# Kernel tuning notes

Measured on AMD Instinct MI355X. Metric: run time of the kernel, lower is better.

## Reference

```python
import jax, jax.numpy as jnp
import numpy as np

B, T, C, D = 4, 20, 128, 64
TD = T * D  # 1280; adaptor input dim = 2*TD = 2560


def setup_inputs() -> dict:
    key = jax.random.key(0)
    ks = jax.random.split(key, 12)

    def lin(k, out_d, in_d):
        return jax.random.normal(k, (out_d, in_d), jnp.float32) / np.float32(np.sqrt(in_d))

    return {
        "h": jax.random.normal(ks[0], (B, T, C, D), jnp.float32),
        "W1": lin(ks[1], 128, 2 * TD), "b1": jnp.zeros((128,), jnp.float32),
        "W2": lin(ks[2], 256, 128),   "b2": jnp.zeros((256,), jnp.float32),
        "W3": lin(ks[3], 64, 256),    "b3": jnp.zeros((64,), jnp.float32),
        "W4": lin(ks[4], 1, 64),      "b4": jnp.zeros((1,), jnp.float32),
        "A_a": jax.random.normal(ks[5], (C, C), jnp.float32) * 0.01,
        "A_m": jax.random.normal(ks[6], (C, C), jnp.float32) * 0.01,
        "W_add": lin(ks[7], D, D), "b_add": jnp.zeros((D,), jnp.float32),
        "W_mod": lin(ks[8], D, D), "b_mod": jnp.zeros((D,), jnp.float32),
        "beta1": jnp.float32(1.0), "beta2": jnp.float32(1.0), "beta3": jnp.float32(1.0),
    }


def reference(h, W1, b1, W2, b2, W3, b3, W4, b4, A_a, A_m,
              W_add, b_add, W_mod, b_mod, beta1, beta2, beta3):
    Bb, Tt, Cc, Dd = h.shape
    td = Tt * Dd
    # H^(u) flattened over time: (B, C, T*D)
    h_flat = jnp.transpose(h, (0, 2, 1, 3)).reshape(Bb, Cc, td)

    # Adaptor MLP on concat(H^u, H^v). First layer is linear on the concat,
    # so split W1 and broadcast-add instead of materializing (B,C,C,2*T*D).
    W1u, W1v = W1[:, :td], W1[:, td:]
    fu = h_flat @ W1u.T                      # (B, C, 128) contribution of u
    fv = h_flat @ W1v.T                      # (B, C, 128) contribution of v
    x = jax.nn.relu(fu[:, :, None, :] + fv[:, None, :, :] + b1)   # (B, Cu, Cv, 128)
    x = jax.nn.relu(jnp.einsum('buvk,mk->buvm', x, W2) + b2)       # (B, Cu, Cv, 256)
    x = jax.nn.relu(jnp.einsum('buvk,mk->buvm', x, W3) + b3)       # (B, Cu, Cv, 64)
    s = jax.nn.sigmoid(jnp.einsum('buvk,mk->buvm', x, W4) + b4)[..., 0]  # (B, C, C)

    # Add path: a_t^(v) = sum_u S^(u,v) * A_a^(u,v) * h_t^(u)
    w = s * A_a[None]                        # (B, Cu, Cv)
    a = jnp.einsum('buv,btud->btvd', w, h)   # (B, T, C, D)
    a = a @ W_add.T + b_add

    # Modulator path: m_t^(v) = (sum_u A_m^(u,v) h_t^(u)) * h_t^(v)
    m = jnp.einsum('uv,btud->btvd', A_m, h) * h
    m = m @ W_mod.T + b_mod

    return beta1 * h + beta2 * a + beta3 * m
```

## Files before the change

kernel.cpp:

```cpp
#include <hip/hip_runtime.h>
#include <cmath>

#define NB 4
#define NT 20
#define NC 128
#define ND 64
#define TD 1280

typedef short short8 __attribute__((ext_vector_type(8)));
typedef float f32x4 __attribute__((ext_vector_type(4)));

static __device__ __forceinline__ unsigned short f2bf(float f) {
  union { float f; unsigned int u; } v; v.f = f;
  unsigned int r = v.u + 0x7FFFu + ((v.u >> 16) & 1u);
  return (unsigned short)(r >> 16);
}

static __device__ __forceinline__ void conv16(const float* __restrict__ s,
                                              unsigned short* __restrict__ d) {
#pragma unroll
  for (int q = 0; q < 2; q++) {
    float4 f0 = *(const float4*)(s + q * 8);
    float4 f1 = *(const float4*)(s + q * 8 + 4);
    uint4 o;
    o.x = (unsigned)f2bf(f0.x) | ((unsigned)f2bf(f0.y) << 16);
    o.y = (unsigned)f2bf(f0.z) | ((unsigned)f2bf(f0.w) << 16);
    o.z = (unsigned)f2bf(f1.x) | ((unsigned)f2bf(f1.y) << 16);
    o.w = (unsigned)f2bf(f1.z) | ((unsigned)f2bf(f1.w) << 16);
    *(uint4*)(d + q * 8) = o;
  }
}

__global__ __launch_bounds__(256) void k_conv_a(
    const float* __restrict__ h, const float* __restrict__ W1,
    unsigned short* __restrict__ hbf, unsigned short* __restrict__ W1bf) {
  int blk = blockIdx.x, tid = threadIdx.x;
  if (blk < 160) {
    int bt = blk >> 1;
    int j = ((blk & 1) << 12) + tid * 16;
    int b = bt / 20;
    int c = j >> 6, d0 = j & 63;
    int t5 = bt - b * 20;
    conv16(h + (size_t)bt * 8192 + j,
           hbf + ((size_t)(b * NC + c)) * TD + t5 * 64 + d0);
  } else {
    size_t i = (size_t)(blk - 160) * 4096 + tid * 16;
    conv16(W1 + i, W1bf + i);
  }
}

__global__ __launch_bounds__(128) void k_fuv2(
    const unsigned short* __restrict__ hbf,
    const unsigned short* __restrict__ W1bf,
    const float* __restrict__ h, const float* __restrict__ W2,
    const float* __restrict__ W3, const float* __restrict__ A_m,
    const float* __restrict__ W_add, const float* __restrict__ W_mod,
    float* __restrict__ fuv,
    unsigned short* __restrict__ W2bf, unsigned short* __restrict__ W3bf,
    unsigned short* __restrict__ A_mTbf, unsigned short* __restrict__ W_addbf,
    unsigned short* __restrict__ W_modbf, unsigned short* __restrict__ hbfT) {
  __shared__ float hsl[128][65];
  int blk = blockIdx.x, tid = threadIdx.x;
  if (blk < 256) {
    int mtile = blk & 15;
    int ntile = blk >> 4;
    int lane = tid & 63;
    int w = tid >> 6;
    int lr = lane & 15, lhi = lane >> 4;
    int row = mtile * 32 + w * 16 + lr;
    const unsigned short* ap = hbf + (size_t)row * TD + lhi * 8;
    int n = ntile * 16 + lr;
    const unsigned short* bp =
        W1bf + (size_t)(n & 127) * (2 * TD) + (n >> 7) * TD + lhi * 8;
    f32x4 acc = (f32x4){0.f, 0.f, 0.f, 0.f};
#pragma unroll 4
    for (int kb = 0; kb < TD; kb += 32) {
      short8 a = *(const short8*)(ap + kb);
      short8 bv = *(const short8*)(bp + kb);
      acc = __builtin_amdgcn_mfma_f32_16x16x32_bf16(a, bv, acc, 0, 0, 0);
    }
    int m0 = mtile * 32 + w * 16 + lhi * 4;
#pragma unroll
    for (int r = 0; r < 4; r++)
      fuv[(size_t)(m0 + r) * 256 + n] = acc[r];
    return;
  }
  int cb = blk - 256;
  if (cb < 16) {
    size_t i = (size_t)cb * 2048 + tid * 16;
    conv16(W2 + i, W2bf + i);
  } else if (cb < 24) {
    size_t i = (size_t)(cb - 16) * 2048 + tid * 16;
    conv16(W3 + i, W3bf + i);
  } else if (cb < 32) {
    size_t base = (size_t)(cb - 24) * 2048 + tid * 16;
    unsigned short tmp[16];
#pragma unroll
    for (int i2 = 0; i2 < 16; i2++) {
      size_t idx = base + i2;
      int v = (int)(idx >> 7), u = (int)(idx & 127);
      tmp[i2] = f2bf(A_m[(size_t)u * 128 + v]);
    }
    *(uint4*)(A_mTbf + base) = *(uint4*)tmp;
    *(uint4*)(A_mTbf + base + 8) = *(uint4*)(tmp + 8);
  } else if (cb < 34) {
    size_t i = (size_t)(cb - 32) * 2048 + tid * 16;
    conv16(W_add + i, W_addbf + i);
  } else if (cb < 36) {
    size_t i = (size_t)(cb - 34) * 2048 + tid * 16;
    conv16(W_mod + i, W_modbf + i);
  } else {
    int bt = cb - 36;
    const float* hb = h + (size_t)bt * 8192;
    for (int i = tid; i < 8192; i += 128) hsl[i >> 6][i & 63] = hb[i];
    __syncthreads();
    unsigned short* ob = hbfT + (size_t)bt * 8192;
    for (int i = tid; i < 8192; i += 128) {
      int d = i >> 7, u = i & 127;
      ob[i] = f2bf(hsl[u][d]);
    }
  }
}

__global__ __launch_bounds__(256) void k_pair(
    const float* __restrict__ fuv, const float* __restrict__ b1,
    const unsigned short* __restrict__ W2bf, const float* __restrict__ b2,
    const unsigned short* __restrict__ W3bf, const float* __restrict__ b3,
    const float* __restrict__ W4, const float* __restrict__ b4,
    const float* __restrict__ A_a, unsigned short* __restrict__ wTbf) {
  int blk = blockIdx.x;
  int b = blk >> 7;
  int u = blk & 127;
  __shared__ char ycraw[4][4096];
  __shared__ char w2c[2][16384];
  __shared__ char w3c[2][8192];
  int t = threadIdx.x;
  int lane = t & 63;
  int w = t >> 6;
  int lr = lane & 15;
  int lhi = lane >> 4;
  int v0w = w * 32;
  int sw = (lr & 7) << 4;

  for (int s = w; s < 16; s += 4) {
    int o = s * 1024 + lane * 16;
    int row = o >> 8;
    int cbo = o & 255;
    const char* src = (const char*)W2bf + (size_t)row * 256 +
                      (cbo ^ ((row & 7) << 4));
    __builtin_amdgcn_global_load_lds(src, w2c[0] + s * 1024, 16, 0, 0);
  }
  for (int s = w; s < 8; s += 4) {
    int o = s * 1024 + lane * 16;
    int row = o >> 7;
    int cbo = o & 127;
    const char* src = (const char*)W3bf + (size_t)row * 512 +
                      (cbo ^ ((row & 7) << 4));
    __builtin_amdgcn_global_load_lds(src, w3c[0] + s * 1024, 16, 0, 0);
  }

  short8 xf[4][2];
  {
    const float* fu_base = fuv + ((size_t)(b * NC + u)) * 256;
#pragma unroll
    for (int ks = 0; ks < 4; ks++) {
      int k0 = ks * 32 + lhi * 8;
      float4 fua = *(const float4*)(fu_base + k0);
      float4 fub4 = *(const float4*)(fu_base + k0 + 4);
      float4 b1a = *(const float4*)(b1 + k0);
      float4 b1b = *(const float4*)(b1 + k0 + 4);
#pragma unroll
      for (int vg = 0; vg < 2; vg++) {
        int v = v0w + vg * 16 + lr;
        const float* fvr = fuv + ((size_t)(b * NC + v)) * 256 + 128 + k0;
        float4 fva = *(const float4*)(fvr);
        float4 fvb = *(const float4*)(fvr + 4);
        float e[8];
        e[0] = fua.x + fva.x + b1a.x; e[1] = fua.y + fva.y + b1a.y;
        e[2] = fua.z + fva.z + b1a.z; e[3] = fua.w + fva.w + b1a.w;
        e[4] = fub4.x + fvb.x + b1b.x; e[5] = fub4.y + fvb.y + b1b.y;
        e[6] = fub4.z + fvb.z + b1b.z; e[7] = fub4.w + fvb.w + b1b.w;
        union { unsigned int pw[4]; short8 s8; } pk;
#pragma unroll
        for (int i2 = 0; i2 < 4; i2++) {
          float lo = e[2 * i2] > 0.f ? e[2 * i2] : 0.f;
          float hi = e[2 * i2 + 1] > 0.f ? e[2 * i2 + 1] : 0.f;
          pk.pw[i2] = (unsigned int)f2bf(lo) | ((unsigned int)f2bf(hi) << 16);
        }
        xf[ks][vg] = pk.s8;
      }
    }
  }
  __syncthreads();

  char* ycb = ycraw[w];
  f32x4 zacc[2][4];
#pragma unroll
  for (int q = 0; q < 2; q++)
#pragma unroll
    for (int n = 0; n < 4; n++) zacc[q][n] = (f32x4){0.f, 0.f, 0.f, 0.f};

  for (int c = 0; c < 4; c++) {
    int mc = c * 64;
    char* w2cur = w2c[c & 1];
    char* w3cur = w3c[c & 1];
    if (c < 3) {
      int mn = mc + 64;
      char* w2nxt = w2c[(c + 1) & 1];
      char* w3nxt = w3c[(c + 1) & 1];
      for (int s = w; s < 16; s += 4) {
        int o = s * 1024 + lane * 16;
        int row = o >> 8;
        int cbo = o & 255;
        const char* src = (const char*)W2bf + (size_t)(mn + row) * 256 +
                          (cbo ^ ((row & 7) << 4));
        __builtin_amdgcn_global_load_lds(src, w2nxt + s * 1024, 16, 0, 0);
      }
      for (int s = w; s < 8; s += 4) {
        int o = s * 1024 + lane * 16;
        int row = o >> 7;
        int cbo = o & 127;
        const char* src = (const char*)W3bf + (size_t)row * 512 + mn * 2 +
                          (cbo ^ ((row & 7) << 4));
        __builtin_amdgcn_global_load_lds(src, w3nxt + s * 1024, 16, 0, 0);
      }
    }

    f32x4 yac[4][2];
#pragma unroll
    for (int mt = 0; mt < 4; mt++) {
      yac[mt][0] = (f32x4){0.f, 0.f, 0.f, 0.f};
      yac[mt][1] = (f32x4){0.f, 0.f, 0.f, 0.f};
    }
    __builtin_amdgcn_s_setprio(1);
#pragma unroll
    for (int ks = 0; ks < 4; ks++) {
#pragma unroll
      for (int mt = 0; mt < 4; mt++) {
        int wrow = mt * 16 + lr;
        short8 wv = *(const short8*)(
            w2cur + wrow * 256 + ((ks * 64 + lhi * 16) ^ ((wrow & 7) << 4)));
        yac[mt][0] = __builtin_amdgcn_mfma_f32_16x16x32_bf16(wv, xf[ks][0], yac[mt][0], 0, 0, 0);
        yac[mt][1] = __builtin_amdgcn_mfma_f32_16x16x32_bf16(wv, xf[ks][1], yac[mt][1], 0, 0, 0);
      }
    }
    __builtin_amdgcn_s_setprio(0);
#pragma unroll
    for (int mt = 0; mt < 4; mt++) {
      float4 b2v = *(const float4*)(b2 + mc + mt * 16 + lhi * 4);
#pragma unroll
      for (int vg = 0; vg < 2; vg++) {
        int v = vg * 16 + lr;
        float e0 = yac[mt][vg][0] + b2v.x; e0 = e0 > 0.f ? e0 : 0.f;
        float e1 = yac[mt][vg][1] + b2v.y; e1 = e1 > 0.f ? e1 : 0.f;
        float e2 = yac[mt][vg][2] + b2v.z; e2 = e2 > 0.f ? e2 : 0.f;
        float e3 = yac[mt][vg][3] + b2v.w; e3 = e3 > 0.f ? e3 : 0.f;
        uint2 pw;
        pw.x = (unsigned)f2bf(e0) | ((unsigned)f2bf(e1) << 16);
        pw.y = (unsigned)f2bf(e2) | ((unsigned)f2bf(e3) << 16);
        int byte = (v * 128 + (mt * 16 + lhi * 4) * 2) ^ ((lr & 7) << 4);
        *(uint2*)(ycb + byte) = pw;
      }
    }
    __builtin_amdgcn_s_setprio(1);
#pragma unroll
    for (int ks2 = 0; ks2 < 2; ks2++) {
      int kb = ks2 * 32 + lhi * 8;
      short8 ya0 = *(const short8*)(ycb + ((lr * 128 + kb * 2) ^ sw));
      short8 ya1 = *(const short8*)(ycb + (((16 + lr) * 128 + kb * 2) ^ sw));
#pragma unroll
      for (int n = 0; n < 4; n++) {
        int jrow = 16 * n + lr;
        short8 w3v = *(const short8*)(
            w3cur + jrow * 128 + ((ks2 * 64 + lhi * 16) ^ ((jrow & 7) << 4)));
        zacc[0][n] = __builtin_amdgcn_mfma_f32_16x16x32_bf16(ya0, w3v, zacc[0][n], 0, 0, 0);
        zacc[1][n] = __builtin_amdgcn_mfma_f32_16x16x32_bf16(ya1, w3v, zacc[1][n], 0, 0, 0);
      }
    }
    __builtin_amdgcn_s_setprio(0);
    __syncthreads();
  }

  float sp[2][4];
#pragma unroll
  for (int q = 0; q < 2; q++)
#pragma unroll
    for (int r = 0; r < 4; r++) sp[q][r] = 0.f;
#pragma unroll
  for (int n = 0; n < 4; n++) {
    int j = 16 * n + lr;
    float b3v = b3[j], w4v = W4[j];
#pragma unroll
    for (int q = 0; q < 2; q++)
#pragma unroll
      for (int r = 0; r < 4; r++) {
        float z = zacc[q][n][r] + b3v;
        z = z > 0.f ? z : 0.f;
        sp[q][r] += w4v * z;
      }
  }
#pragma unroll
  for (int mask = 1; mask <= 8; mask <<= 1)
#pragma unroll
    for (int q = 0; q < 2; q++)
#pragma unroll
      for (int r = 0; r < 4; r++)
        sp[q][r] += __shfl_xor(sp[q][r], mask, 64);
  float bb4 = b4[0];
  if (lr == 0) {
#pragma unroll
    for (int q = 0; q < 2; q++)
#pragma unroll
      for (int r = 0; r < 4; r++) {
        int v = v0w + 16 * q + lhi * 4 + r;
        float s = 1.f / (1.f + expf(-(sp[q][r] + bb4)));
        wTbf[((size_t)(b * NC + v)) * NC + u] = f2bf(s * A_a[u * NC + v]);
      }
  }
}

__global__ __launch_bounds__(128) void k_out_mfma(
    const float* __restrict__ h, const unsigned short* __restrict__ wTbf,
    const unsigned short* __restrict__ A_mTbf,
    const unsigned short* __restrict__ hbfT,
    const unsigned short* __restrict__ W_addbf,
    const unsigned short* __restrict__ W_modbf,
    const float* __restrict__ b_add, const float* __restrict__ b_mod,
    const float* __restrict__ beta1p, const float* __restrict__ beta2p,
    const float* __restrict__ beta3p, float* __restrict__ out) {
  int blk = blockIdx.x;
  int bt = blk >> 3;
  int v0 = (blk & 7) << 4;
  int b = bt / 20;
  __shared__ char apre_l[2048];
  __shared__ char mpre_l[2048];
  int t = threadIdx.x;
  int lane = t & 63;
  int w = t >> 6;
  int lr = lane & 15, lhi = lane >> 4;
  int nf0 = w * 2;

  f32x4 aacc[2], macc[2];
#pragma unroll
  for (int i = 0; i < 2; i++) {
    aacc[i] = (f32x4){0.f, 0.f, 0.f, 0.f};
    macc[i] = (f32x4){0.f, 0.f, 0.f, 0.f};
  }
  const unsigned short* wrow = wTbf + ((size_t)(b * NC + v0 + lr)) * NC + lhi * 8;
  const unsigned short* arow = A_mTbf + (size_t)(v0 + lr) * NC + lhi * 8;
  const unsigned short* hTrow = hbfT + (size_t)bt * 8192 + lhi * 8;
#pragma unroll
  for (int kb = 0; kb < 128; kb += 32) {
    short8 aw = *(const short8*)(wrow + kb);
    short8 am = *(const short8*)(arow + kb);
#pragma unroll
    for (int nfi = 0; nfi < 2; nfi++) {
      int nf = nf0 + nfi;
      short8 bv = *(const short8*)(hTrow + (size_t)(nf * 16 + lr) * NC + kb);
      aacc[nfi] = __builtin_amdgcn_mfma_f32_16x16x32_bf16(aw, bv, aacc[nfi], 0, 0, 0);
      macc[nfi] = __builtin_amdgcn_mfma_f32_16x16x32_bf16(am, bv, macc[nfi], 0, 0, 0);
    }
  }

  float hval[2][4];
  const float* hbase = h + (size_t)bt * 8192;
#pragma unroll
  for (int nfi = 0; nfi < 2; nfi++) {
    int d = (nf0 + nfi) * 16 + lr;
#pragma unroll
    for (int r = 0; r < 4; r++) {
      int vl = lhi * 4 + r;
      float hv = hbase[(size_t)(v0 + vl) * 64 + d];
      hval[nfi][r] = hv;
      int byte = (vl * 128 + d * 2) ^ ((vl & 7) << 4);
      *(unsigned short*)(apre_l + byte) = f2bf(aacc[nfi][r]);
      *(unsigned short*)(mpre_l + byte) = f2bf(macc[nfi][r] * hv);
    }
  }
  __syncthreads();

  f32x4 oa[2], om[2];
#pragma unroll
  for (int i = 0; i < 2; i++) {
    oa[i] = (f32x4){0.f, 0.f, 0.f, 0.f};
    om[i] = (f32x4){0.f, 0.f, 0.f, 0.f};
  }
  int sw = (lr & 7) << 4;
#pragma unroll
  for (int kb = 0; kb < 64; kb += 32) {
    int off0 = lr * 128 + kb * 2 + lhi * 16;
    short8 pa = *(const short8*)(apre_l + (off0 ^ sw));
    short8 pm = *(const short8*)(mpre_l + (off0 ^ sw));
#pragma unroll
    for (int nfi = 0; nfi < 2; nfi++) {
      int nf = nf0 + nfi;
      const unsigned short* wa = W_addbf + (size_t)(nf * 16 + lr) * 64 + kb + lhi * 8;
      const unsigned short* wm = W_modbf + (size_t)(nf * 16 + lr) * 64 + kb + lhi * 8;
      short8 wav = *(const short8*)wa;
      short8 wmv = *(const short8*)wm;
      oa[nfi] = __builtin_amdgcn_mfma_f32_16x16x32_bf16(pa, wav, oa[nfi], 0, 0, 0);
      om[nfi] = __builtin_amdgcn_mfma_f32_16x16x32_bf16(pm, wmv, om[nfi], 0, 0, 0);
    }
  }
  float bb1 = beta1p[0], bb2 = beta2p[0], bb3 = beta3p[0];
  float* obase = out + (size_t)bt * 8192 + (size_t)v0 * 64;
#pragma unroll
  for (int nfi = 0; nfi < 2; nfi++) {
    int d = (nf0 + nfi) * 16 + lr;
    float ba = b_add[d], bm = b_mod[d];
#pragma unroll
    for (int r = 0; r < 4; r++) {
      int vl = lhi * 4 + r;
      obase[(size_t)vl * 64 + d] =
          bb1 * hval[nfi][r] + bb2 * (oa[nfi][r] + ba) + bb3 * (om[nfi][r] + bm);
    }
  }
}

extern "C" void kernel_launch(void* const* d_in, const int* in_sizes, int n_in,
                              void* d_out, int out_size, void* d_ws, size_t ws_size,
                              hipStream_t stream) {
  const float* h     = (const float*)d_in[0];
  const float* W1    = (const float*)d_in[1];
  const float* b1    = (const float*)d_in[2];
  const float* W2    = (const float*)d_in[3];
  const float* b2    = (const float*)d_in[4];
  const float* W3    = (const float*)d_in[5];
  const float* b3    = (const float*)d_in[6];
  const float* W4    = (const float*)d_in[7];
  const float* b4    = (const float*)d_in[8];
  const float* A_a   = (const float*)d_in[9];
  const float* A_m   = (const float*)d_in[10];
  const float* W_add = (const float*)d_in[11];
  const float* b_add = (const float*)d_in[12];
  const float* W_mod = (const float*)d_in[13];
  const float* b_mod = (const float*)d_in[14];
  const float* beta1 = (const float*)d_in[15];
  const float* beta2 = (const float*)d_in[16];
  const float* beta3 = (const float*)d_in[17];
  float* out = (float*)d_out;

  char* ws = (char*)d_ws;
  float* fuv             = (float*)(ws);
  unsigned short* wTbf   = (unsigned short*)(ws + 512 * 1024);
  unsigned short* A_mTbf = (unsigned short*)(ws + 640 * 1024);
  unsigned short* W_addbf= (unsigned short*)(ws + 672 * 1024);
  unsigned short* W_modbf= (unsigned short*)(ws + 680 * 1024);
  unsigned short* W2bf   = (unsigned short*)(ws + 688 * 1024);
  unsigned short* W3bf   = (unsigned short*)(ws + 752 * 1024);
  unsigned short* W1bf   = (unsigned short*)(ws + 784 * 1024);
  unsigned short* hbf    = (unsigned short*)(ws + 1424 * 1024);
  unsigned short* hbfT   = (unsigned short*)(ws + 2704 * 1024);

  k_conv_a<<<240, 256, 0, stream>>>(h, W1, hbf, W1bf);
  k_fuv2<<<372, 128, 0, stream>>>(hbf, W1bf, h, W2, W3, A_m, W_add, W_mod,
                                  fuv, W2bf, W3bf, A_mTbf, W_addbf, W_modbf,
                                  hbfT);
  k_pair<<<512, 256, 0, stream>>>(fuv, b1, W2bf, b2, W3bf, b3, W4, b4, A_a, wTbf);
  k_out_mfma<<<640, 128, 0, stream>>>(h, wTbf, A_mTbf, hbfT, W_addbf, W_modbf,
                                      b_add, b_mod, beta1, beta2, beta3, out);
}
```

Before: 43.90 us.

## Fuse bf16 conversion of h and W1 into fuv GEMM via swizzled LDS tiles

Removes the separate k_conv_a kernel that wrote bf16 copies of h and W1 to global memory. The fuv GEMM blocks now load fp32 h and W1 directly, convert them to bf16 and stage 128-wide K chunks in XOR-swizzled shared memory before the MFMA steps. This saves a kernel launch and a global write/read round trip, but each GEMM block redoes the conversion and adds two barriers per K chunk with no double buffering.

```diff
diff --git a/kernel.cpp b/kernel.cpp
--- a/kernel.cpp
+++ b/kernel.cpp
@@ -31,55 +31,83 @@
   }
 }
 
-__global__ __launch_bounds__(256) void k_conv_a(
+static __device__ __forceinline__ void conv16_lds(const float* __restrict__ s,
+                                                  char* __restrict__ base,
+                                                  int byte0, int swz) {
+#pragma unroll
+  for (int q = 0; q < 2; q++) {
+    float4 f0 = *(const float4*)(s + q * 8);
+    float4 f1 = *(const float4*)(s + q * 8 + 4);
+    uint4 o;
+    o.x = (unsigned)f2bf(f0.x) | ((unsigned)f2bf(f0.y) << 16);
+    o.y = (unsigned)f2bf(f0.z) | ((unsigned)f2bf(f0.w) << 16);
+    o.z = (unsigned)f2bf(f1.x) | ((unsigned)f2bf(f1.y) << 16);
+    o.w = (unsigned)f2bf(f1.z) | ((unsigned)f2bf(f1.w) << 16);
+    *(uint4*)(base + ((byte0 + q * 16) ^ swz)) = o;
+  }
+}
+
+__global__ __launch_bounds__(128) void k_front2(
     const float* __restrict__ h, const float* __restrict__ W1,
-    unsigned short* __restrict__ hbf, unsigned short* __restrict__ W1bf) {
-  int blk = blockIdx.x, tid = threadIdx.x;
-  if (blk < 160) {
-    int bt = blk >> 1;
-    int j = ((blk & 1) << 12) + tid * 16;
-    int b = bt / 20;
-    int c = j >> 6, d0 = j & 63;
-    int t5 = bt - b * 20;
-    conv16(h + (size_t)bt * 8192 + j,
-           hbf + ((size_t)(b * NC + c)) * TD + t5 * 64 + d0);
-  } else {
-    size_t i = (size_t)(blk - 160) * 4096 + tid * 16;
-    conv16(W1 + i, W1bf + i);
-  }
-}
-
-__global__ __launch_bounds__(128) void k_fuv2(
-    const unsigned short* __restrict__ hbf,
-    const unsigned short* __restrict__ W1bf,
-    const float* __restrict__ h, const float* __restrict__ W2,
-    const float* __restrict__ W3, const float* __restrict__ A_m,
-    const float* __restrict__ W_add, const float* __restrict__ W_mod,
+    const float* __restrict__ W2, const float* __restrict__ W3,
+    const float* __restrict__ A_m, const float* __restrict__ W_add,
+    const float* __restrict__ W_mod,
     float* __restrict__ fuv,
     unsigned short* __restrict__ W2bf, unsigned short* __restrict__ W3bf,
     unsigned short* __restrict__ A_mTbf, unsigned short* __restrict__ W_addbf,
     unsigned short* __restrict__ W_modbf, unsigned short* __restrict__ hbfT) {
-  __shared__ float hsl[128][65];
+  __shared__ char smem[33280];
   int blk = blockIdx.x, tid = threadIdx.x;
   if (blk < 256) {
+    char* atile = smem;
+    char* btile = smem + 8192;
     int mtile = blk & 15;
     int ntile = blk >> 4;
     int lane = tid & 63;
     int w = tid >> 6;
     int lr = lane & 15, lhi = lane >> 4;
-    int row = mtile * 32 + w * 16 + lr;
-    const unsigned short* ap = hbf + (size_t)row * TD + lhi * 8;
+    int ac = tid >> 2;
+    int akseg = (tid & 3) << 5;
+    int arow_g = mtile * 32 + ac;
+    int ab = arow_g >> 7, acc_c = arow_g & 127;
+    int aswz = (ac & 7) << 4;
+    int abase = ac * 256 + akseg * 2;
+    int bn = tid >> 3;
+    int bkseg = (tid & 7) << 4;
+    int bn_g = ntile * 16 + bn;
+    const float* bsrc_row =
+        W1 + (size_t)(bn_g & 127) * (2 * TD) + (bn_g >> 7) * TD;
+    int bswz = (bn & 7) << 4;
+    int bbase = bn * 256 + bkseg * 2;
+    int arow_l = w * 16 + lr;
+    int a_rd_base = arow_l * 256;
+    int a_rd_swz = (lr & 7) << 4;
+    int b_rd_base = lr * 256;
+
+    f32x4 acc = (f32x4){0.f, 0.f, 0.f, 0.f};
+    for (int kc = 0; kc < 10; kc++) {
+      int k0 = kc * 128;
+      if (kc) __syncthreads();
+      {
+        int t5 = (k0 + akseg) >> 6;
+        int d0 = akseg & 63;
+        const float* src =
+            h + (((size_t)(ab * NT + t5)) * NC + acc_c) * ND + d0;
+        conv16_lds(src, atile, abase, aswz);
+        conv16_lds(src + 16, atile, abase + 32, aswz);
+      }
+      conv16_lds(bsrc_row + k0 + bkseg, btile, bbase, bswz);
+      __syncthreads();
+#pragma unroll
+      for (int ks = 0; ks < 4; ks++) {
+        int koff = ks * 64 + lhi * 16;
+        short8 a = *(const short8*)(atile + a_rd_base + (koff ^ a_rd_swz));
+        short8 bv = *(const short8*)(btile + b_rd_base + (koff ^ ((lr & 7) << 4)));
+        acc = __builtin_amdgcn_mfma_f32_16x16x32_bf16(a, bv, acc, 0, 0, 0);
+      }
+    }
+    int m0 = mtile * 32 + w * 16 + lhi * 4;
     int n = ntile * 16 + lr;
-    const unsigned short* bp =
-        W1bf + (size_t)(n & 127) * (2 * TD) + (n >> 7) * TD + lhi * 8;
-    f32x4 acc = (f32x4){0.f, 0.f, 0.f, 0.f};
-#pragma unroll 4
-    for (int kb = 0; kb < TD; kb += 32) {
-      short8 a = *(const short8*)(ap + kb);
-      short8 bv = *(const short8*)(bp + kb);
-      acc = __builtin_amdgcn_mfma_f32_16x16x32_bf16(a, bv, acc, 0, 0, 0);
-    }
-    int m0 = mtile * 32 + w * 16 + lhi * 4;
 #pragma unroll
     for (int r = 0; r < 4; r++)
       fuv[(size_t)(m0 + r) * 256 + n] = acc[r];
@@ -110,6 +138,7 @@
     size_t i = (size_t)(cb - 34) * 2048 + tid * 16;
     conv16(W_mod + i, W_modbf + i);
   } else {
+    float (*hsl)[65] = (float (*)[65])smem;
     int bt = cb - 36;
     const float* hb = h + (size_t)bt * 8192;
     for (int i = tid; i < 8192; i += 128) hsl[i >> 6][i & 63] = hb[i];
@@ -448,14 +477,11 @@
   unsigned short* W_modbf= (unsigned short*)(ws + 680 * 1024);
   unsigned short* W2bf   = (unsigned short*)(ws + 688 * 1024);
   unsigned short* W3bf   = (unsigned short*)(ws + 752 * 1024);
-  unsigned short* W1bf   = (unsigned short*)(ws + 784 * 1024);
-  unsigned short* hbf    = (unsigned short*)(ws + 1424 * 1024);
-  unsigned short* hbfT   = (unsigned short*)(ws + 2704 * 1024);
-
-  k_conv_a<<<240, 256, 0, stream>>>(h, W1, hbf, W1bf);
-  k_fuv2<<<372, 128, 0, stream>>>(hbf, W1bf, h, W2, W3, A_m, W_add, W_mod,
-                                  fuv, W2bf, W3bf, A_mTbf, W_addbf, W_modbf,
-                                  hbfT);
+  unsigned short* hbfT   = (unsigned short*)(ws + 784 * 1024);
+
+  k_front2<<<372, 128, 0, stream>>>(h, W1, W2, W3, A_m, W_add, W_mod,
+                                    fuv, W2bf, W3bf, A_mTbf, W_addbf, W_modbf,
+                                    hbfT);
   k_pair<<<512, 256, 0, stream>>>(fuv, b1, W2bf, b2, W3bf, b3, W4, b4, A_a, wTbf);
   k_out_mfma<<<640, 128, 0, stream>>>(h, wTbf, A_mTbf, hbfT, W_addbf, W_modbf,
                                       b_add, b_mod, beta1, beta2, beta3, out);
```

Result: faster. 42.66 us (-2.8%).
